# Performance work log

Hardware: AMD Instinct MI355X
Metric: run time of the kernel (lower is better)

The kernel has to match this reference:

```python
import jax, jax.numpy as jnp
import numpy as np

M1, M2, M3 = 16, 16, 3  # Fourier mode truncation (modes3 hard-coded to 3 in torch __init__)


def setup_inputs() -> dict:
    key = jax.random.key(0)
    k0, k1, k2, k3, k4 = jax.random.split(key, 5)
    B, Ci, Co, T, X, P = 8, 32, 32, 128, 256, 3
    scale = 1.0 / (Ci * Co)
    x = jax.random.normal(k0, (B, Ci, T, X, P), dtype=jnp.float32)
    w1_re = scale * jax.random.uniform(k1, (Ci, Co, M1, M2, M3), dtype=jnp.float32)
    w1_im = scale * jax.random.uniform(k2, (Ci, Co, M1, M2, M3), dtype=jnp.float32)
    w2_re = scale * jax.random.uniform(k3, (Ci, Co, M1, M2, M3), dtype=jnp.float32)
    w2_im = scale * jax.random.uniform(k4, (Ci, Co, M1, M2, M3), dtype=jnp.float32)
    return {"x": x, "w1_re": w1_re, "w1_im": w1_im, "w2_re": w2_re, "w2_im": w2_im}


def reference(x, w1_re, w1_im, w2_re, w2_im):
    # x: [B, Ci, T, X, P] -- pipes pre-stacked along last dim (method == 34 branch)
    B, Ci, T, X, P = x.shape
    Co = w1_re.shape[1]
    w1 = (w1_re + 1j * w1_im).astype(jnp.complex64)
    w2 = (w2_re + 1j * w2_im).astype(jnp.complex64)

    x_ft = jnp.fft.rfftn(x, axes=(2, 3, 4))          # [B, Ci, T, X, P//2+1]
    z = min(x_ft.shape[4], M3)                       # torch: z_dim = min(x_ft.shape[4], modes3)

    # low-x / low-y corner
    coeff1 = jnp.zeros((B, Ci, M1, M2, M3), jnp.complex64)
    coeff1 = coeff1.at[..., :z].set(x_ft[:, :, :M1, :M2, :z])
    blk1 = jnp.einsum('bixyz,ioxyz->boxyz', coeff1, w1)

    # high-x / low-y corner
    coeff2 = jnp.zeros((B, Ci, M1, M2, M3), jnp.complex64)
    coeff2 = coeff2.at[..., :z].set(x_ft[:, :, -M1:, :M2, :z])
    blk2 = jnp.einsum('bixyz,ioxyz->boxyz', coeff2, w2)

    out_ft = jnp.zeros((B, Co, T, X, P), jnp.complex64)
    out_ft = out_ft.at[:, :, :M1, :M2, :M3].set(blk1)
    out_ft = out_ft.at[:, :, -M1:, :M2, :M3].set(blk2)

    # irfftn with s=(T, X, P) crops last axis to P//2+1 coeffs, matching torch semantics
    out = jnp.fft.irfftn(out_ft, s=(T, X, P), axes=(-3, -2, -1))  # [B, Co, T, X, P] float32
    return out
```

## Files before the change

kernel.cpp:

```cpp
#include <hip/hip_runtime.h>
#include <math.h>

typedef float2 F2;

__device__ __forceinline__ F2 cmul(F2 a, F2 b) {
    return make_float2(a.x * b.x - a.y * b.y, a.x * b.y + a.y * b.x);
}
__device__ __forceinline__ F2 cmac(F2 acc, F2 a, F2 b) {
    acc.x += a.x * b.x - a.y * b.y;
    acc.y += a.x * b.y + a.y * b.x;
    return acc;
}

#define TWO_PI 6.283185307179586f
#define SQRT3_2 0.8660254037844386f
#define SQRT3 1.7320508075688772f

__global__ __launch_bounds__(256) void k1_fwd_x(const float* __restrict__ x,
                                                F2* __restrict__ y) {
    __shared__ float xp0[8][257];
    __shared__ F2    xp1[8][257];
    const int tid = threadIdx.x;
    const int blk = blockIdx.x;

#pragma unroll
    for (int j = 0; j < 8; ++j) {
        int item = tid + 256 * j;
        int row = item >> 8, xx = item & 255;
        const float* src = x + ((size_t)(blk * 8 + row) * 256 + xx) * 3;
        float a = src[0], b = src[1], c = src[2];
        xp0[row][xx] = a + b + c;
        xp1[row][xx] = make_float2(a - 0.5f * (b + c), SQRT3_2 * (c - b));
    }
    __syncthreads();

    const int kz = tid >> 7, rr = (tid >> 4) & 7, kx = tid & 15;
    const float sgn = (kx & 1) ? -1.0f : 1.0f;
    F2 w = make_float2(1.f, 0.f), step;
    sincosf(-TWO_PI * (float)kx * (1.0f / 256.0f), &step.y, &step.x);
    F2 acc = make_float2(0.f, 0.f);
    if (kz == 0) {
        for (int xx = 0; xx < 128; ++xx) {
            float s = xp0[rr][xx] + sgn * xp0[rr][xx + 128];
            acc.x += s * w.x;
            acc.y += s * w.y;
            w = cmul(w, step);
        }
    } else {
        for (int xx = 0; xx < 128; ++xx) {
            F2 a = xp1[rr][xx], b = xp1[rr][xx + 128];
            F2 s = make_float2(a.x + sgn * b.x, a.y + sgn * b.y);
            acc = cmac(acc, s, w);
            w = cmul(w, step);
        }
    }
    const int row_g = blk * 8 + rr;
    y[((size_t)row_g * 2 + kz) * 16 + kx] = acc;
}

__global__ __launch_bounds__(256) void k2a_fwd_t(const F2* __restrict__ y,
                                                 F2* __restrict__ xft) {
    __shared__ F2 yL[128][16];
    const int tid = threadIdx.x;
    const int bi = blockIdx.x >> 1, kz = blockIdx.x & 1;
#pragma unroll
    for (int j = 0; j < 8; ++j) {
        int item = tid + 256 * j;
        int t = item >> 4, kx = item & 15;
        yL[t][kx] = y[((size_t)(bi * 128 + t) * 2 + kz) * 16 + kx];
    }
    __syncthreads();

    const int kx = tid & 15, sg = tid >> 4;
    F2 rotA = make_float2(1.f, 0.f), rotB = make_float2(1.f, 0.f), stepA, stepB;
    sincosf(-TWO_PI * (float)sg * (1.0f / 128.0f), &stepA.y, &stepA.x);
    sincosf(-TWO_PI * (float)(112 + sg) * (1.0f / 128.0f), &stepB.y, &stepB.x);
    F2 accA = make_float2(0.f, 0.f), accB = make_float2(0.f, 0.f);
    for (int t = 0; t < 128; ++t) {
        F2 v = yL[t][kx];
        accA = cmac(accA, v, rotA);
        accB = cmac(accB, v, rotB);
        rotA = cmul(rotA, stepA);
        rotB = cmul(rotB, stepB);
    }
    const int b = bi >> 5, i = bi & 31;
    xft[(((size_t)(b * 32 + sg) * 2 + kz) * 16 + kx) * 32 + i] = accA;
    xft[(((size_t)(b * 32 + (16 + sg)) * 2 + kz) * 16 + kx) * 32 + i] = accB;
}

__global__ __launch_bounds__(256) void k2b_mix(const F2* __restrict__ xft,
                                               const float* __restrict__ w1re,
                                               const float* __restrict__ w1im,
                                               const float* __restrict__ w2re,
                                               const float* __restrict__ w2im,
                                               F2* __restrict__ blkout) {
    __shared__ F2 xL[512];
    __shared__ float wr[2][32][32];
    __shared__ float wi[2][32][32];
    const int tid = threadIdx.x;
    const int s = blockIdx.x >> 4, kx = blockIdx.x & 15;
#pragma unroll
    for (int j = 0; j < 2; ++j) {
        int item = tid + 256 * j;
        int b = item >> 6, kz = (item >> 5) & 1, i = item & 31;
        xL[item] = xft[(((size_t)(b * 32 + s) * 2 + kz) * 16 + kx) * 32 + i];
    }
    const float* bre = (s < 16) ? w1re : w2re;
    const float* bim = (s < 16) ? w1im : w2im;
    const int m1 = s & 15;
#pragma unroll
    for (int j = 0; j < 4; ++j) {
        int iop = tid + 256 * j;
        int i = iop >> 5, o = iop & 31;
        size_t g = (((size_t)(i * 32 + o) * 16 + m1) * 16 + kx) * 3;
        wr[0][i][o] = bre[g];
        wr[1][i][o] = bre[g + 1];
        wi[0][i][o] = bim[g];
        wi[1][i][o] = bim[g + 1];
    }
    __syncthreads();

    const int b = tid >> 5, o = tid & 31;
#pragma unroll
    for (int kz = 0; kz < 2; ++kz) {
        F2 acc = make_float2(0.f, 0.f);
        for (int i = 0; i < 32; ++i) {
            F2 xv = xL[(b * 2 + kz) * 32 + i];
            float wrv = wr[kz][i][o], wiv = wi[kz][i][o];
            acc.x += xv.x * wrv - xv.y * wiv;
            acc.y += xv.x * wiv + xv.y * wrv;
        }
        blkout[(((size_t)(b * 32 + o) * 32 + s) * 2 + kz) * 16 + kx] = acc;
    }
}

__global__ __launch_bounds__(256) void k2c_inv_t(const F2* __restrict__ blkin,
                                                 F2* __restrict__ h) {
    __shared__ F2 bL[1024];
    const int tid = threadIdx.x;
    const int bo = blockIdx.x;
#pragma unroll
    for (int j = 0; j < 4; ++j) {
        int item = tid + 256 * j;
        bL[item] = blkin[(size_t)bo * 1024 + item];
    }
    __syncthreads();

    const int col = tid & 31, tg = tid >> 5;
    F2 accA[16], accB[16], w[16], stp[16];
#pragma unroll
    for (int jj = 0; jj < 16; ++jj) {
        accA[jj] = make_float2(0.f, 0.f);
        accB[jj] = make_float2(0.f, 0.f);
        w[jj] = make_float2(1.f, 0.f);
        int t = tg + 8 * jj;
        sincosf(TWO_PI * (float)t * (1.0f / 128.0f), &stp[jj].y, &stp[jj].x);
    }
    for (int sp = 0; sp < 16; ++sp) {
        F2 bA = bL[sp * 32 + col];
        F2 bB = bL[(16 + sp) * 32 + col];
#pragma unroll
        for (int jj = 0; jj < 16; ++jj) {
            accA[jj] = cmac(accA[jj], bA, w[jj]);
            accB[jj] = cmac(accB[jj], bB, w[jj]);
            w[jj] = cmul(w[jj], stp[jj]);
        }
    }
    F2 phase;
    sincosf(-TWO_PI * (float)tg * (1.0f / 8.0f), &phase.y, &phase.x);
#pragma unroll
    for (int jj = 0; jj < 16; ++jj) {
        int t = tg + 8 * jj;
        F2 r = cmac(accA[jj], phase, accB[jj]);
        h[((size_t)bo * 128 + t) * 32 + col] = r;
    }
}

__global__ __launch_bounds__(256) void k3_inv_x(const F2* __restrict__ h,
                                                float* __restrict__ out) {
    __shared__ F2 hL[64];
    const int tid = threadIdx.x;
    const int blk = blockIdx.x;
    if (tid < 64) hL[tid] = h[(size_t)blk * 64 + tid];
    __syncthreads();

    const int rr = tid >> 7, x = tid & 127;
    const F2* hrow = &hL[rr * 32];
    F2 w = make_float2(1.f, 0.f), r;
    sincosf(TWO_PI * (float)x * (1.0f / 256.0f), &r.y, &r.x);
    float e0 = 0.f, o0 = 0.f;
    F2 e1 = make_float2(0.f, 0.f), o1 = make_float2(0.f, 0.f);
#pragma unroll
    for (int k2 = 0; k2 < 8; ++k2) {
        {
            F2 h0 = hrow[2 * k2], h1 = hrow[16 + 2 * k2];
            e0 += h0.x * w.x - h0.y * w.y;
            e1.x += h1.x * w.x - h1.y * w.y;
            e1.y += h1.x * w.y + h1.y * w.x;
            w = cmul(w, r);
        }
        {
            F2 h0 = hrow[2 * k2 + 1], h1 = hrow[16 + 2 * k2 + 1];
            o0 += h0.x * w.x - h0.y * w.y;
            o1.x += h1.x * w.x - h1.y * w.y;
            o1.y += h1.x * w.y + h1.y * w.x;
            w = cmul(w, r);
        }
    }
    const float n = 1.0f / 98304.0f;
    float* dst = out + ((size_t)blk * 2 + rr) * 768;
    {
        float g0 = e0 + o0, g1r = e1.x + o1.x, g1i = e1.y + o1.y;
        dst[x * 3 + 0] = n * (g0 + 2.f * g1r);
        dst[x * 3 + 1] = n * (g0 - g1r - SQRT3 * g1i);
        dst[x * 3 + 2] = n * (g0 - g1r + SQRT3 * g1i);
    }
    {
        float g0 = e0 - o0, g1r = e1.x - o1.x, g1i = e1.y - o1.y;
        int xb = x + 128;
        dst[xb * 3 + 0] = n * (g0 + 2.f * g1r);
        dst[xb * 3 + 1] = n * (g0 - g1r - SQRT3 * g1i);
        dst[xb * 3 + 2] = n * (g0 - g1r + SQRT3 * g1i);
    }
}

extern "C" void kernel_launch(void* const* d_in, const int* in_sizes, int n_in,
                              void* d_out, int out_size, void* d_ws, size_t ws_size,
                              hipStream_t stream) {
    const float* x    = (const float*)d_in[0];
    const float* w1re = (const float*)d_in[1];
    const float* w1im = (const float*)d_in[2];
    const float* w2re = (const float*)d_in[3];
    const float* w2im = (const float*)d_in[4];
    float* out = (float*)d_out;

    F2* y   = (F2*)d_ws;
    F2* xft = y + 1048576;
    F2* bk  = xft + 262144;
    F2* h   = bk + 262144;

    hipLaunchKernelGGL(k1_fwd_x,  dim3(4096),  dim3(256), 0, stream, x, y);
    hipLaunchKernelGGL(k2a_fwd_t, dim3(512),   dim3(256), 0, stream, y, xft);
    hipLaunchKernelGGL(k2b_mix,   dim3(512),   dim3(256), 0, stream, xft,
                       w1re, w1im, w2re, w2im, bk);
    hipLaunchKernelGGL(k2c_inv_t, dim3(256),   dim3(256), 0, stream, bk, h);
    hipLaunchKernelGGL(k3_inv_x,  dim3(16384), dim3(256), 0, stream, h, out);
}
```

Baseline: 268.1 us.

## Register-block forward x-DFT, interleave complex weights, split inverse-t kernel across blocks

The forward x-direction DFT kernel now gives each thread 4 output frequencies and a strided quarter of the input samples. Twiddles are seeded from a shared-memory table and partial sums are reduced through shared memory, so the serial 128-step dependent loop becomes a 32-step loop with four independent chains. The mixing kernel stores weights as interleaved complex pairs to halve the shared loads per multiply. The inverse-t kernel is split four ways over output time, so it launches four times as many blocks with a quarter of the registers each. This adds extra syncs and a reduction step in the first kernel, and the inverse-t kernel now reloads its input block four times.

```diff
diff --git a/kernel.cpp b/kernel.cpp
--- a/kernel.cpp
+++ b/kernel.cpp
@@ -20,9 +20,16 @@
                                                 F2* __restrict__ y) {
     __shared__ float xp0[8][257];
     __shared__ F2    xp1[8][257];
+    __shared__ F2    tw[256];
+    __shared__ F2    part[1024];
     const int tid = threadIdx.x;
     const int blk = blockIdx.x;
 
+    {
+        float sv, cv;
+        sincosf(-TWO_PI * (float)tid * (1.0f / 256.0f), &sv, &cv);
+        tw[tid] = make_float2(cv, sv);
+    }
 #pragma unroll
     for (int j = 0; j < 8; ++j) {
         int item = tid + 256 * j;
@@ -34,28 +41,60 @@
     }
     __syncthreads();
 
-    const int kz = tid >> 7, rr = (tid >> 4) & 7, kx = tid & 15;
-    const float sgn = (kx & 1) ? -1.0f : 1.0f;
-    F2 w = make_float2(1.f, 0.f), step;
-    sincosf(-TWO_PI * (float)kx * (1.0f / 256.0f), &step.y, &step.x);
-    F2 acc = make_float2(0.f, 0.f);
+    const int kz = tid >> 7, rr = (tid >> 4) & 7, kxg = (tid >> 2) & 3, c = tid & 3;
+    const float sgn = (kxg & 1) ? -1.0f : 1.0f;
+
+    F2 acc[4], w[4], stp[4];
+#pragma unroll
+    for (int u = 0; u < 4; ++u) {
+        int kx = kxg + 4 * u;
+        acc[u] = make_float2(0.f, 0.f);
+        w[u] = tw[(kx * c) & 255];
+        stp[u] = tw[(4 * kx) & 255];
+    }
+
     if (kz == 0) {
-        for (int xx = 0; xx < 128; ++xx) {
-            float s = xp0[rr][xx] + sgn * xp0[rr][xx + 128];
-            acc.x += s * w.x;
-            acc.y += s * w.y;
-            w = cmul(w, step);
+        const float* r0 = xp0[rr];
+#pragma unroll 8
+        for (int m = 0; m < 32; ++m) {
+            int xx = c + 4 * m;
+            float s = fmaf(sgn, r0[xx + 128], r0[xx]);
+#pragma unroll
+            for (int u = 0; u < 4; ++u) {
+                acc[u].x = fmaf(s, w[u].x, acc[u].x);
+                acc[u].y = fmaf(s, w[u].y, acc[u].y);
+                w[u] = cmul(w[u], stp[u]);
+            }
         }
     } else {
-        for (int xx = 0; xx < 128; ++xx) {
-            F2 a = xp1[rr][xx], b = xp1[rr][xx + 128];
-            F2 s = make_float2(a.x + sgn * b.x, a.y + sgn * b.y);
-            acc = cmac(acc, s, w);
-            w = cmul(w, step);
-        }
-    }
-    const int row_g = blk * 8 + rr;
-    y[((size_t)row_g * 2 + kz) * 16 + kx] = acc;
+        const F2* r1 = xp1[rr];
+#pragma unroll 8
+        for (int m = 0; m < 32; ++m) {
+            int xx = c + 4 * m;
+            F2 a = r1[xx], b = r1[xx + 128];
+            F2 s = make_float2(fmaf(sgn, b.x, a.x), fmaf(sgn, b.y, a.y));
+#pragma unroll
+            for (int u = 0; u < 4; ++u) {
+                acc[u] = cmac(acc[u], s, w[u]);
+                w[u] = cmul(w[u], stp[u]);
+            }
+        }
+    }
+
+#pragma unroll
+    for (int u = 0; u < 4; ++u) {
+        int kx = kxg + 4 * u;
+        part[(((rr * 2 + kz) * 16 + kx) << 2) + c] = acc[u];
+    }
+    __syncthreads();
+    {
+        int rr2 = tid >> 5, kz2 = (tid >> 4) & 1, kx2 = tid & 15;
+        const F2* p = &part[((rr2 * 2 + kz2) * 16 + kx2) << 2];
+        F2 r = p[0];
+        r.x += p[1].x + p[2].x + p[3].x;
+        r.y += p[1].y + p[2].y + p[3].y;
+        y[((size_t)(blk * 8 + rr2) * 2 + kz2) * 16 + kx2] = r;
+    }
 }
 
 __global__ __launch_bounds__(256) void k2a_fwd_t(const F2* __restrict__ y,
@@ -95,8 +134,7 @@
                                                const float* __restrict__ w2im,
                                                F2* __restrict__ blkout) {
     __shared__ F2 xL[512];
-    __shared__ float wr[2][32][32];
-    __shared__ float wi[2][32][32];
+    __shared__ F2 wcL[2][32][32];
     const int tid = threadIdx.x;
     const int s = blockIdx.x >> 4, kx = blockIdx.x & 15;
 #pragma unroll
@@ -113,10 +151,8 @@
         int iop = tid + 256 * j;
         int i = iop >> 5, o = iop & 31;
         size_t g = (((size_t)(i * 32 + o) * 16 + m1) * 16 + kx) * 3;
-        wr[0][i][o] = bre[g];
-        wr[1][i][o] = bre[g + 1];
-        wi[0][i][o] = bim[g];
-        wi[1][i][o] = bim[g + 1];
+        wcL[0][i][o] = make_float2(bre[g], bim[g]);
+        wcL[1][i][o] = make_float2(bre[g + 1], bim[g + 1]);
     }
     __syncthreads();
 
@@ -126,9 +162,9 @@
         F2 acc = make_float2(0.f, 0.f);
         for (int i = 0; i < 32; ++i) {
             F2 xv = xL[(b * 2 + kz) * 32 + i];
-            float wrv = wr[kz][i][o], wiv = wi[kz][i][o];
-            acc.x += xv.x * wrv - xv.y * wiv;
-            acc.y += xv.x * wiv + xv.y * wrv;
+            F2 wv = wcL[kz][i][o];
+            acc.x += xv.x * wv.x - xv.y * wv.y;
+            acc.y += xv.x * wv.y + xv.y * wv.x;
         }
         blkout[(((size_t)(b * 32 + o) * 32 + s) * 2 + kz) * 16 + kx] = acc;
     }
@@ -138,7 +174,7 @@
                                                  F2* __restrict__ h) {
     __shared__ F2 bL[1024];
     const int tid = threadIdx.x;
-    const int bo = blockIdx.x;
+    const int bo = blockIdx.x >> 2, tc = blockIdx.x & 3;
 #pragma unroll
     for (int j = 0; j < 4; ++j) {
         int item = tid + 256 * j;
@@ -146,32 +182,32 @@
     }
     __syncthreads();
 
-    const int col = tid & 31, tg = tid >> 5;
-    F2 accA[16], accB[16], w[16], stp[16];
-#pragma unroll
-    for (int jj = 0; jj < 16; ++jj) {
-        accA[jj] = make_float2(0.f, 0.f);
-        accB[jj] = make_float2(0.f, 0.f);
-        w[jj] = make_float2(1.f, 0.f);
-        int t = tg + 8 * jj;
-        sincosf(TWO_PI * (float)t * (1.0f / 128.0f), &stp[jj].y, &stp[jj].x);
+    const int col = tid & 31, tl = tid >> 5;
+    F2 accA[4], accB[4], w[4], stp[4];
+#pragma unroll
+    for (int q = 0; q < 4; ++q) {
+        accA[q] = make_float2(0.f, 0.f);
+        accB[q] = make_float2(0.f, 0.f);
+        w[q] = make_float2(1.f, 0.f);
+        int t = 32 * tc + tl + 8 * q;
+        sincosf(TWO_PI * (float)t * (1.0f / 128.0f), &stp[q].y, &stp[q].x);
     }
     for (int sp = 0; sp < 16; ++sp) {
         F2 bA = bL[sp * 32 + col];
         F2 bB = bL[(16 + sp) * 32 + col];
 #pragma unroll
-        for (int jj = 0; jj < 16; ++jj) {
-            accA[jj] = cmac(accA[jj], bA, w[jj]);
-            accB[jj] = cmac(accB[jj], bB, w[jj]);
-            w[jj] = cmul(w[jj], stp[jj]);
+        for (int q = 0; q < 4; ++q) {
+            accA[q] = cmac(accA[q], bA, w[q]);
+            accB[q] = cmac(accB[q], bB, w[q]);
+            w[q] = cmul(w[q], stp[q]);
         }
     }
     F2 phase;
-    sincosf(-TWO_PI * (float)tg * (1.0f / 8.0f), &phase.y, &phase.x);
-#pragma unroll
-    for (int jj = 0; jj < 16; ++jj) {
-        int t = tg + 8 * jj;
-        F2 r = cmac(accA[jj], phase, accB[jj]);
+    sincosf(-TWO_PI * (float)tl * (1.0f / 8.0f), &phase.y, &phase.x);
+#pragma unroll
+    for (int q = 0; q < 4; ++q) {
+        int t = 32 * tc + tl + 8 * q;
+        F2 r = cmac(accA[q], phase, accB[q]);
         h[((size_t)bo * 128 + t) * 32 + col] = r;
     }
 }
@@ -243,6 +279,6 @@
     hipLaunchKernelGGL(k2a_fwd_t, dim3(512),   dim3(256), 0, stream, y, xft);
     hipLaunchKernelGGL(k2b_mix,   dim3(512),   dim3(256), 0, stream, xft,
                        w1re, w1im, w2re, w2im, bk);
-    hipLaunchKernelGGL(k2c_inv_t, dim3(256),   dim3(256), 0, stream, bk, h);
+    hipLaunchKernelGGL(k2c_inv_t, dim3(1024),  dim3(256), 0, stream, bk, h);
     hipLaunchKernelGGL(k3_inv_x,  dim3(16384), dim3(256), 0, stream, h, out);
 }
```

After: 264.0 us. About the same (-1.5%).
